# Kernel optimization log

Hardware: AMD Instinct MI355X
Metric: run time of the kernel (lower is better)

The kernel has to match this reference:

```python
import jax, jax.numpy as jnp
import numpy as np

HEAD_DIM = 128
NUM_HEADS = 16
CONTEXT_LENGTH = 4096
THETA_BASE = 10000.0


def precompute_rope(head_dim, context_length, theta_base=THETA_BASE):
    inv_freq = 1.0 / theta_base ** (jnp.arange(0, head_dim, 2, dtype=jnp.float32) / head_dim)
    positions = jnp.arange(context_length, dtype=jnp.float32)
    angles = positions[:, None] * inv_freq[None, :]          # [T, hd/2]
    angles = jnp.concatenate([angles, angles], axis=1)       # [T, hd]
    return jnp.cos(angles), jnp.sin(angles)


def apply_rope(x, cos, sin):
    # x: [b, h, s, hd]
    s, hd = x.shape[2], x.shape[3]
    x1, x2 = x[..., : hd // 2], x[..., hd // 2 :]
    rotated = jnp.concatenate([-x2, x1], axis=-1)
    return (x * cos[None, None, :s, :] + rotated * sin[None, None, :s, :]).astype(x.dtype)


def setup_inputs() -> dict:
    key = jax.random.key(0)
    ks = jax.random.split(key, 5)
    b, s, d = 2, 2048, 2048
    scale = 1.0 / np.sqrt(d)
    return {
        "x": jax.random.normal(ks[0], (b, s, d), dtype=jnp.float32),
        "Wq": jax.random.normal(ks[1], (d, d), dtype=jnp.float32) * scale,
        "Wk": jax.random.normal(ks[2], (d, d), dtype=jnp.float32) * scale,
        "Wv": jax.random.normal(ks[3], (d, d), dtype=jnp.float32) * scale,
        "Wo": jax.random.normal(ks[4], (d, d), dtype=jnp.float32) * scale,
    }


def reference(x, Wq, Wk, Wv, Wo):
    b, s, d = x.shape
    h, hd = NUM_HEADS, HEAD_DIM
    cos, sin = precompute_rope(hd, CONTEXT_LENGTH)

    q = (x @ Wq).reshape(b, s, h, hd).transpose(0, 2, 1, 3)  # [b,h,s,hd]
    k = (x @ Wk).reshape(b, s, h, hd).transpose(0, 2, 1, 3)
    v = (x @ Wv).reshape(b, s, h, hd).transpose(0, 2, 1, 3)

    q = apply_rope(q, cos, sin)
    k = apply_rope(k, cos, sin)

    scores = jnp.einsum("bhqd,bhkd->bhqk", q, k)             # [b,h,s,s]
    causal = jnp.tril(jnp.ones((s, s), dtype=bool))
    scores = jnp.where(causal[None, None], scores, -jnp.inf)
    weights = jax.nn.softmax(scores / np.sqrt(hd), axis=-1)
    ctx = jnp.einsum("bhqk,bhkd->bhqd", weights, v)          # [b,h,s,hd]
    ctx = ctx.transpose(0, 2, 1, 3).reshape(b, s, d)
    return ctx @ Wo
```

## Files before the change

### kernel.cpp

```cpp
#include <hip/hip_runtime.h>
#include <hip/hip_bf16.h>

typedef __attribute__((ext_vector_type(8))) __bf16 bf16x8;
typedef __attribute__((ext_vector_type(8))) short  short8;
typedef __attribute__((ext_vector_type(4))) float  f32x4;
typedef unsigned short u16;
typedef unsigned int   u32;

__device__ __forceinline__ u16 f2bf(float f) {
  u32 u = __builtin_bit_cast(u32, f);
  u += 0x7fffu + ((u >> 16) & 1u);
  return (u16)(u >> 16);
}
__device__ __forceinline__ float bf2f(u16 h) {
  return __builtin_bit_cast(float, (u32)h << 16);
}

#define MFMA_BF16(a, b, c) __builtin_amdgcn_mfma_f32_16x16x32_bf16( \
    __builtin_bit_cast(bf16x8, (a)), __builtin_bit_cast(bf16x8, (b)), (c), 0, 0, 0)

__device__ __forceinline__ void gload_lds16(const void* g, void* l) {
  __builtin_amdgcn_global_load_lds(
      (const __attribute__((address_space(1))) void*)g,
      (__attribute__((address_space(3))) void*)l, 16, 0, 0);
}

#define SEQ   2048
#define DMODEL 2048
#define NH    16
#define HD    128

static constexpr size_t SZ_MAT   = 4096ull * 2048 * 2;
static constexpr size_t OFF_XB   = 0;
static constexpr size_t OFF_WQKVT= OFF_XB   + SZ_MAT;
static constexpr size_t OFF_WOT  = OFF_WQKVT+ 3ull*2048*2048*2;
static constexpr size_t OFF_Q    = OFF_WOT  + 2048ull*2048*2;
static constexpr size_t OFF_K    = OFF_Q    + SZ_MAT;
static constexpr size_t OFF_VT   = OFF_K    + SZ_MAT;
static constexpr size_t OFF_CTX  = OFF_VT   + SZ_MAT;
static constexpr size_t OFF_COS  = OFF_CTX  + SZ_MAT;
static constexpr size_t OFF_SIN  = OFF_COS  + 2048ull*64*4;
static constexpr size_t WS_NEED  = OFF_SIN  + 2048ull*64*4;

__global__ void cast_x_kernel(const float* __restrict__ x, u16* __restrict__ xb, int n4) {
  int id = blockIdx.x * blockDim.x + threadIdx.x;
  if (id >= n4) return;
  float4 v = ((const float4*)x)[id];
  ushort4 o;
  o.x = f2bf(v.x); o.y = f2bf(v.y); o.z = f2bf(v.z); o.w = f2bf(v.w);
  ((ushort4*)xb)[id] = o;
}

__global__ void castT_w_kernel(const float* __restrict__ W0, const float* __restrict__ W1,
                               const float* __restrict__ W2, const float* __restrict__ W3,
                               u16* __restrict__ Wqkvt, u16* __restrict__ Wot) {
  __shared__ float tile[32][33];
  int z = blockIdx.z;
  const float* W = (z == 0) ? W0 : (z == 1) ? W1 : (z == 2) ? W2 : W3;
  u16* Out = (z < 3) ? (Wqkvt + (size_t)z * 2048 * 2048) : Wot;
  int n0 = blockIdx.x * 32, k0 = blockIdx.y * 32;
  int tx = threadIdx.x, ty = threadIdx.y;
  #pragma unroll
  for (int i = 0; i < 4; i++)
    tile[ty + 8 * i][tx] = W[(size_t)(k0 + ty + 8 * i) * 2048 + n0 + tx];
  __syncthreads();
  #pragma unroll
  for (int i = 0; i < 4; i++)
    Out[(size_t)(n0 + ty + 8 * i) * 2048 + k0 + tx] = f2bf(tile[tx][ty + 8 * i]);
}

__global__ void rope_table_kernel(float* __restrict__ ct, float* __restrict__ st) {
  int id = blockIdx.x * blockDim.x + threadIdx.x;
  int pos = id >> 6, j = id & 63;
  float inv = exp2f(-(float)j * (13.287712379549449f / 64.0f));
  float a = (float)pos * inv;
  ct[id] = cosf(a);
  st[id] = sinf(a);
}

__global__ void rope_apply_kernel(u16* __restrict__ Q, u16* __restrict__ K,
                                  const float* __restrict__ ct, const float* __restrict__ st) {
  int id = blockIdx.x * blockDim.x + threadIdx.x;
  u16* P = blockIdx.y ? K : Q;
  int row = id >> 10;
  int r = id & 1023;
  int hh = r >> 6, j = r & 63;
  int pos = row & 2047;
  size_t base = (size_t)row * 2048 + hh * 128 + j;
  float x1 = bf2f(P[base]), x2 = bf2f(P[base + 64]);
  float c = ct[pos * 64 + j], s = st[pos * 64 + j];
  P[base]      = f2bf(x1 * c - x2 * s);
  P[base + 64] = f2bf(x2 * c + x1 * s);
}

template <int EPI>
__global__ __launch_bounds__(256)
void gemm_bt_kernel(const u16* __restrict__ A, const u16* __restrict__ Bt,
                    u16* __restrict__ Qo, u16* __restrict__ Ko, u16* __restrict__ Vto,
                    float* __restrict__ Co, int K) {
  __shared__ u16 Al[128 * 32];
  __shared__ u16 Bl[128 * 32];
  const int tid = threadIdx.x;
  const int lane = tid & 63;
  const int w = tid >> 6;
  const int grp = lane >> 4, lr = lane & 15;
  const int bm = blockIdx.y, bn = blockIdx.x;
  const int wm = w >> 1, wn = w & 1;
  f32x4 acc[4][4] = {};
  const char* Ab = (const char*)(A + (size_t)bm * 128 * K);
  const char* Bb = (const char*)(Bt + (size_t)bn * 128 * K);
  const int c0 = tid, c1 = tid + 256;
  const int rA0 = c0 >> 2, cb0 = (c0 & 3) * 16;
  const int rA1 = c1 >> 2, cb1 = (c1 & 3) * 16;

  for (int kt = 0; kt < K; kt += 32) {
    gload_lds16(Ab + (size_t)rA0 * K * 2 + kt * 2 + cb0, (char*)Al + c0 * 16);
    gload_lds16(Ab + (size_t)rA1 * K * 2 + kt * 2 + cb1, (char*)Al + c1 * 16);
    gload_lds16(Bb + (size_t)rA0 * K * 2 + kt * 2 + cb0, (char*)Bl + c0 * 16);
    gload_lds16(Bb + (size_t)rA1 * K * 2 + kt * 2 + cb1, (char*)Bl + c1 * 16);
    __syncthreads();
    short8 af[4], bf[4];
    #pragma unroll
    for (int mi = 0; mi < 4; mi++)
      af[mi] = *(const short8*)(Al + (wm * 64 + mi * 16 + lr) * 32 + grp * 8);
    #pragma unroll
    for (int nj = 0; nj < 4; nj++)
      bf[nj] = *(const short8*)(Bl + (wn * 64 + nj * 16 + lr) * 32 + grp * 8);
    #pragma unroll
    for (int mi = 0; mi < 4; mi++)
      #pragma unroll
      for (int nj = 0; nj < 4; nj++)
        acc[mi][nj] = MFMA_BF16(af[mi], bf[nj], acc[mi][nj]);
    __syncthreads();
  }

  const int rowBase = bm * 128 + wm * 64 + grp * 4;
  if (EPI == 0) {
    const int seg = bn >> 4;
    const int colBase = (bn & 15) * 128 + wn * 64 + lr;
    if (seg < 2) {
      u16* O = seg ? Ko : Qo;
      #pragma unroll
      for (int mi = 0; mi < 4; mi++)
        #pragma unroll
        for (int nj = 0; nj < 4; nj++) {
          int col = colBase + nj * 16;
          int row = rowBase + mi * 16;
          #pragma unroll
          for (int r = 0; r < 4; r++)
            O[(size_t)(row + r) * 2048 + col] = f2bf(acc[mi][nj][r]);
        }
    } else {
      #pragma unroll
      for (int mi = 0; mi < 4; mi++) {
        int row = rowBase + mi * 16;
        int b = row >> 11, s = row & 2047;
        int sp = (s & ~31) | (((s >> 2) & 3) << 3) | (((s >> 4) & 1) << 2);
        #pragma unroll
        for (int nj = 0; nj < 4; nj++) {
          int colv = colBase + nj * 16;
          ushort4 o;
          o.x = f2bf(acc[mi][nj][0]); o.y = f2bf(acc[mi][nj][1]);
          o.z = f2bf(acc[mi][nj][2]); o.w = f2bf(acc[mi][nj][3]);
          *(ushort4*)(Vto + (size_t)(b * 2048 + colv) * 2048 + sp) = o;
        }
      }
    }
  } else {
    const int colBase = bn * 128 + wn * 64 + lr;
    #pragma unroll
    for (int mi = 0; mi < 4; mi++)
      #pragma unroll
      for (int nj = 0; nj < 4; nj++)
        #pragma unroll
        for (int r = 0; r < 4; r++)
          Co[(size_t)(rowBase + mi * 16 + r) * 2048 + colBase + nj * 16] = acc[mi][nj][r];
  }
}

__global__ __launch_bounds__(512, 4)
void attn_kernel(const u16* __restrict__ Q, const u16* __restrict__ K,
                 const u16* __restrict__ Vt, u16* __restrict__ ctx) {
  __shared__ u16 Kl[2][64 * 128];
  __shared__ u16 Vl[2][128 * 64];
  const int qt = blockIdx.x, bh = blockIdx.y;
  const int b = bh >> 4, h = bh & 15;
  const int tid = threadIdx.x;
  const int w = tid >> 6, lane = tid & 63;
  const int grp = lane >> 4, lr = lane & 15;
  const int q0w = qt * 128 + w * 16;
  const int qrow = q0w + lr;
  const u16* Qp = Q + ((size_t)(b * 2048 + qrow)) * 2048 + h * 128;
  short8 qf[4];
  #pragma unroll
  for (int kk = 0; kk < 4; kk++)
    qf[kk] = *(const short8*)(Qp + kk * 32 + grp * 8);

  f32x4 acc_o[8] = {};
  float m_run = -3.0e38f, l_run = 0.0f;
  const float ce = 0.08838834764831845f * 1.4426950408889634f;

  const char* Kbh = (const char*)K  + ((size_t)b * 2048 * 2048 + h * 128) * 2;
  const char* Vbh = (const char*)Vt + ((size_t)(b * 2048 + h * 128)) * 2048 * 2;

  auto stage = [&](int buf, int kvt) {
    const int kv0 = kvt * 64;
    #pragma unroll
    for (int u = 0; u < 2; u++) {
      int c = tid + u * 512;
      int row = c >> 4, slot = c & 15;
      gload_lds16(Kbh + (size_t)(kv0 + row) * 4096 + ((slot ^ (row & 7)) << 4),
                  (char*)Kl[buf] + c * 16);
    }
    #pragma unroll
    for (int u = 0; u < 2; u++) {
      int c = tid + u * 512;
      int dd = c >> 3, slot = c & 7;
      gload_lds16(Vbh + (size_t)dd * 4096 + kv0 * 2 + ((slot ^ (dd & 7)) << 4),
                  (char*)Vl[buf] + c * 16);
    }
  };

  const int nkv = 2 * qt + 2;
  stage(0, 0);
  __syncthreads();

  for (int kvt = 0; kvt < nkv; kvt++) {
    const int kv0 = kvt * 64;
    const int cur = kvt & 1;
    if (kvt + 1 < nkv) stage(cur ^ 1, kvt + 1);

    if (kv0 <= q0w + 15) {
      const char* Kc = (const char*)Kl[cur];
      const char* Vc = (const char*)Vl[cur];
      f32x4 sa[4] = {};
      #pragma unroll
      for (int kk = 0; kk < 4; kk++) {
        #pragma unroll
        for (int mi = 0; mi < 4; mi++) {
          const int krow = mi * 16 + lr;
          short8 kf = *(const short8*)(Kc + krow * 256 + (((kk * 4 + grp) ^ (krow & 7)) << 4));
          sa[mi] = MFMA_BF16(kf, qf[kk], sa[mi]);
        }
      }
      float tmax = -3.0e38f;
      const bool dg = (kv0 + 63 > qrow);
      #pragma unroll
      for (int mi = 0; mi < 4; mi++)
        #pragma unroll
        for (int r = 0; r < 4; r++) {
          float s = sa[mi][r];
          if (dg && (kv0 + mi * 16 + grp * 4 + r > qrow)) s = -3.0e38f;
          sa[mi][r] = s;
          tmax = fmaxf(tmax, s);
        }
      tmax = fmaxf(tmax, __shfl_xor(tmax, 16, 64));
      tmax = fmaxf(tmax, __shfl_xor(tmax, 32, 64));
      const float m_new = fmaxf(m_run, tmax);
      const float alpha = exp2f((m_run - m_new) * ce);
      float psum = 0.0f;
      #pragma unroll
      for (int mi = 0; mi < 4; mi++)
        #pragma unroll
        for (int r = 0; r < 4; r++) {
          float e = exp2f((sa[mi][r] - m_new) * ce);
          sa[mi][r] = e;
          psum += e;
        }
      psum += __shfl_xor(psum, 16, 64);
      psum += __shfl_xor(psum, 32, 64);
      l_run = l_run * alpha + psum;
      m_run = m_new;
      #pragma unroll
      for (int mi = 0; mi < 8; mi++) acc_o[mi] *= alpha;

      short8 pb[2];
      #pragma unroll
      for (int kb = 0; kb < 2; kb++)
        #pragma unroll
        for (int i = 0; i < 4; i++) {
          pb[kb][i]     = (short)f2bf(sa[2 * kb][i]);
          pb[kb][4 + i] = (short)f2bf(sa[2 * kb + 1][i]);
        }
      #pragma unroll
      for (int mi = 0; mi < 8; mi++) {
        const int vrow = mi * 16 + lr;
        #pragma unroll
        for (int kb = 0; kb < 2; kb++) {
          short8 vf = *(const short8*)(Vc + vrow * 128 + (((kb * 4 + grp) ^ (vrow & 7)) << 4));
          acc_o[mi] = MFMA_BF16(vf, pb[kb], acc_o[mi]);
        }
      }
    }
    __syncthreads();
  }

  const float inv_l = 1.0f / l_run;
  u16* Cp = ctx + ((size_t)(b * 2048 + qrow)) * 2048 + h * 128;
  #pragma unroll
  for (int mi = 0; mi < 8; mi++) {
    ushort4 o;
    o.x = f2bf(acc_o[mi][0] * inv_l);
    o.y = f2bf(acc_o[mi][1] * inv_l);
    o.z = f2bf(acc_o[mi][2] * inv_l);
    o.w = f2bf(acc_o[mi][3] * inv_l);
    *(ushort4*)(Cp + mi * 16 + grp * 4) = o;
  }
}

extern "C" void kernel_launch(void* const* d_in, const int* in_sizes, int n_in,
                              void* d_out, int out_size, void* d_ws, size_t ws_size,
                              hipStream_t stream) {
  const float* x  = (const float*)d_in[0];
  const float* Wq = (const float*)d_in[1];
  const float* Wk = (const float*)d_in[2];
  const float* Wv = (const float*)d_in[3];
  const float* Wo = (const float*)d_in[4];
  float* out = (float*)d_out;
  char* ws = (char*)d_ws;
  if (ws_size < WS_NEED) return;

  u16* xb    = (u16*)(ws + OFF_XB);
  u16* Wqkvt = (u16*)(ws + OFF_WQKVT);
  u16* Wot   = (u16*)(ws + OFF_WOT);
  u16* Qb    = (u16*)(ws + OFF_Q);
  u16* Kb    = (u16*)(ws + OFF_K);
  u16* Vtb   = (u16*)(ws + OFF_VT);
  u16* ctxb  = (u16*)(ws + OFF_CTX);
  float* ctab = (float*)(ws + OFF_COS);
  float* stab = (float*)(ws + OFF_SIN);

  cast_x_kernel<<<8192, 256, 0, stream>>>(x, xb, 2097152);
  castT_w_kernel<<<dim3(64, 64, 4), dim3(32, 8), 0, stream>>>(Wq, Wk, Wv, Wo, Wqkvt, Wot);
  rope_table_kernel<<<512, 256, 0, stream>>>(ctab, stab);
  gemm_bt_kernel<0><<<dim3(48, 32), 256, 0, stream>>>(xb, Wqkvt, Qb, Kb, Vtb, nullptr, 2048);
  rope_apply_kernel<<<dim3(16384, 2), 256, 0, stream>>>(Qb, Kb, ctab, stab);
  attn_kernel<<<dim3(16, 32), 512, 0, stream>>>(Qb, Kb, Vtb, ctxb);
  gemm_bt_kernel<1><<<dim3(16, 32), 256, 0, stream>>>(ctxb, Wot, nullptr, nullptr, nullptr, out, 2048);
}
```

Baseline: 463.9 us.

## Replace QKV projection GEMM with 256x256 double-buffered, swizzled 8-wave kernel

Adds a dedicated QKV GEMM using 256x256 block tiles, 512 threads, a 64-wide K step, XOR-swizzled LDS layout and double-buffered async global-to-LDS loads interleaved with MFMA phases under explicit barriers, vmcnt waits and priority hints. This is meant to raise data reuse and hide memory latency compared with the old 128x128 single-buffered tile that synchronised on every 32-wide K step. The output GEMM keeps the old kernel with the epilogue template removed. The trade-offs are a larger LDS footprint (128KB per block) and a grid of 384 blocks, which may leave the GPU unevenly loaded.

After: 445.2 us. 1.04x faster.

```diff
diff --git a/kernel.cpp b/kernel.cpp
--- a/kernel.cpp
+++ b/kernel.cpp
@@ -93,10 +93,152 @@
   P[base + 64] = f2bf(x2 * c + x1 * s);
 }
 
-template <int EPI>
+#define SB __builtin_amdgcn_sched_barrier(0)
+#define BAR()   do { SB; __builtin_amdgcn_s_barrier(); SB; } while (0)
+#define VMCNT4() do { SB; asm volatile("s_waitcnt vmcnt(4)" ::: "memory"); SB; } while (0)
+#define VMCNT0() do { SB; asm volatile("s_waitcnt vmcnt(0)" ::: "memory"); SB; } while (0)
+
+#define STAGE8(gb, kt, H, lb)                                                  \
+  do { _Pragma("unroll")                                                       \
+    for (int u = 0; u < 2; u++) {                                              \
+      int c = tid + u * 512;                                                   \
+      int rr = c >> 3, sl = c & 7;                                             \
+      gload_lds16((gb) + (size_t)((H) * 128 + rr) * 4096 + (size_t)(kt) * 128  \
+                       + ((sl ^ (rr & 7)) << 4),                               \
+                  (lb) + (H) * 16384 + c * 16);                                \
+    } } while (0)
+
+#define LDA8(lb, MG)                                                           \
+  do { _Pragma("unroll")                                                       \
+    for (int mi = 0; mi < 4; mi++) {                                           \
+      af[mi][0] = *(const short8*)((lb) + aoff + ((MG) + mi) * 2048 + sw0);    \
+      af[mi][1] = *(const short8*)((lb) + aoff + ((MG) + mi) * 2048 + sw1);    \
+    } } while (0)
+
+#define LDB4(lb, NG)                                                           \
+  do { _Pragma("unroll")                                                       \
+    for (int nj = 0; nj < 2; nj++) {                                           \
+      bfr[(NG) + nj][0] = *(const short8*)((lb) + boff + ((NG) + nj) * 2048 + sw0); \
+      bfr[(NG) + nj][1] = *(const short8*)((lb) + boff + ((NG) + nj) * 2048 + sw1); \
+    } } while (0)
+
+#define MMQ(MG, NG)                                                            \
+  do {                                                                         \
+    __builtin_amdgcn_s_setprio(1);                                             \
+    _Pragma("unroll")                                                          \
+    for (int mi = 0; mi < 4; mi++) {                                           \
+      _Pragma("unroll")                                                        \
+      for (int nj = 0; nj < 2; nj++) {                                         \
+        acc[(MG) + mi][(NG) + nj] =                                            \
+            MFMA_BF16(af[mi][0], bfr[(NG) + nj][0], acc[(MG) + mi][(NG) + nj]);\
+        acc[(MG) + mi][(NG) + nj] =                                            \
+            MFMA_BF16(af[mi][1], bfr[(NG) + nj][1], acc[(MG) + mi][(NG) + nj]);\
+      }                                                                        \
+    }                                                                          \
+    __builtin_amdgcn_s_setprio(0);                                             \
+  } while (0)
+
+#define GEMM8_ITER(K1v, K2v, K3v, LAST)                                        \
+  do {                                                                         \
+    LDA8(A0p, 0); LDB4(B0p, 0);                                                \
+    STAGE8(Ab, (K1v), 0, A1p);                                                 \
+    BAR(); MMQ(0, 0); BAR();                                                   \
+    LDB4(B0p, 2);                                                              \
+    STAGE8(Ab, (K1v), 1, A1p);                                                 \
+    BAR(); MMQ(0, 2); BAR();                                                   \
+    LDA8(A0p, 4);                                                              \
+    if (!(LAST)) STAGE8(Bb, (K2v), 0, B0p);                                    \
+    BAR(); MMQ(4, 2); BAR();                                                   \
+    if (!(LAST)) STAGE8(Ab, (K2v), 0, A0p);                                    \
+    if (LAST) { VMCNT0(); } else { VMCNT4(); }                                 \
+    BAR(); MMQ(4, 0); BAR();                                                   \
+    LDA8(A1p, 0); LDB4(B1p, 0);                                                \
+    if (!(LAST)) STAGE8(Ab, (K2v), 1, A0p);                                    \
+    BAR(); MMQ(0, 0); BAR();                                                   \
+    LDB4(B1p, 2);                                                              \
+    if (!(LAST)) STAGE8(Bb, (K2v), 1, B0p);                                    \
+    BAR(); MMQ(0, 2); BAR();                                                   \
+    LDA8(A1p, 4);                                                              \
+    if (!(LAST)) STAGE8(Bb, (K3v), 0, B1p);                                    \
+    BAR(); MMQ(4, 2); BAR();                                                   \
+    if (!(LAST)) { STAGE8(Bb, (K3v), 1, B1p); VMCNT4(); }                      \
+    BAR(); MMQ(4, 0); BAR();                                                   \
+  } while (0)
+
+__global__ __launch_bounds__(512, 2)
+void gemm8_qkv_kernel(const u16* __restrict__ A, const u16* __restrict__ Bt,
+                      u16* __restrict__ Qo, u16* __restrict__ Ko,
+                      u16* __restrict__ Vto) {
+  __shared__ u16 Asm[2][16384];
+  __shared__ u16 Bsm[2][16384];
+  const int tid = threadIdx.x;
+  const int lane = tid & 63, w = tid >> 6;
+  const int grp = lane >> 4, lr = lane & 15;
+  const int wm = w >> 2, wn = w & 3;
+  const int bm = blockIdx.y, bn = blockIdx.x;
+
+  const char* Ab = (const char*)A + (size_t)bm * 256 * 4096;
+  const char* Bb = (const char*)Bt + (size_t)bn * 256 * 4096;
+  char* A0p = (char*)Asm[0]; char* A1p = (char*)Asm[1];
+  char* B0p = (char*)Bsm[0]; char* B1p = (char*)Bsm[1];
+
+  f32x4 acc[8][4] = {};
+  short8 af[4][2], bfr[4][2];
+  const int aoff = wm * 16384 + lr * 128;
+  const int boff = wn * 8192 + lr * 128;
+  const int sw0 = ((grp    ) ^ (lr & 7)) << 4;
+  const int sw1 = ((grp + 4) ^ (lr & 7)) << 4;
+
+  STAGE8(Ab, 0, 0, A0p);
+  STAGE8(Ab, 0, 1, A0p);
+  STAGE8(Bb, 0, 0, B0p);
+  STAGE8(Bb, 0, 1, B0p);
+  STAGE8(Bb, 1, 0, B1p);
+  STAGE8(Bb, 1, 1, B1p);
+  VMCNT4();
+  BAR();
+
+  #pragma unroll 1
+  for (int t = 0; t < 15; ++t) {
+    GEMM8_ITER(2 * t + 1, 2 * t + 2, 2 * t + 3, false);
+  }
+  GEMM8_ITER(31, 0, 0, true);
+
+  const int seg = bn >> 3;
+  const int row0 = bm * 256 + wm * 128 + grp * 4;
+  const int col0 = (bn & 7) * 256 + wn * 64 + lr;
+  if (seg < 2) {
+    u16* O = seg ? Ko : Qo;
+    #pragma unroll
+    for (int ai = 0; ai < 8; ai++)
+      #pragma unroll
+      for (int nj = 0; nj < 4; nj++) {
+        int col = col0 + nj * 16;
+        int row = row0 + ai * 16;
+        #pragma unroll
+        for (int r = 0; r < 4; r++)
+          O[(size_t)(row + r) * 2048 + col] = f2bf(acc[ai][nj][r]);
+      }
+  } else {
+    #pragma unroll
+    for (int ai = 0; ai < 8; ai++) {
+      int row = row0 + ai * 16;
+      int b = row >> 11, s = row & 2047;
+      int sp = (s & ~31) | (((s >> 2) & 3) << 3) | (((s >> 4) & 1) << 2);
+      #pragma unroll
+      for (int nj = 0; nj < 4; nj++) {
+        int colv = col0 + nj * 16;
+        ushort4 o;
+        o.x = f2bf(acc[ai][nj][0]); o.y = f2bf(acc[ai][nj][1]);
+        o.z = f2bf(acc[ai][nj][2]); o.w = f2bf(acc[ai][nj][3]);
+        *(ushort4*)(Vto + (size_t)(b * 2048 + colv) * 2048 + sp) = o;
+      }
+    }
+  }
+}
+
 __global__ __launch_bounds__(256)
 void gemm_bt_kernel(const u16* __restrict__ A, const u16* __restrict__ Bt,
-                    u16* __restrict__ Qo, u16* __restrict__ Ko, u16* __restrict__ Vto,
                     float* __restrict__ Co, int K) {
   __shared__ u16 Al[128 * 32];
   __shared__ u16 Bl[128 * 32];
@@ -135,47 +277,14 @@
   }
 
   const int rowBase = bm * 128 + wm * 64 + grp * 4;
-  if (EPI == 0) {
-    const int seg = bn >> 4;
-    const int colBase = (bn & 15) * 128 + wn * 64 + lr;
-    if (seg < 2) {
-      u16* O = seg ? Ko : Qo;
-      #pragma unroll
-      for (int mi = 0; mi < 4; mi++)
-        #pragma unroll
-        for (int nj = 0; nj < 4; nj++) {
-          int col = colBase + nj * 16;
-          int row = rowBase + mi * 16;
-          #pragma unroll
-          for (int r = 0; r < 4; r++)
-            O[(size_t)(row + r) * 2048 + col] = f2bf(acc[mi][nj][r]);
-        }
-    } else {
-      #pragma unroll
-      for (int mi = 0; mi < 4; mi++) {
-        int row = rowBase + mi * 16;
-        int b = row >> 11, s = row & 2047;
-        int sp = (s & ~31) | (((s >> 2) & 3) << 3) | (((s >> 4) & 1) << 2);
-        #pragma unroll
-        for (int nj = 0; nj < 4; nj++) {
-          int colv = colBase + nj * 16;
-          ushort4 o;
-          o.x = f2bf(acc[mi][nj][0]); o.y = f2bf(acc[mi][nj][1]);
-          o.z = f2bf(acc[mi][nj][2]); o.w = f2bf(acc[mi][nj][3]);
-          *(ushort4*)(Vto + (size_t)(b * 2048 + colv) * 2048 + sp) = o;
-        }
-      }
-    }
-  } else {
-    const int colBase = bn * 128 + wn * 64 + lr;
-    #pragma unroll
-    for (int mi = 0; mi < 4; mi++)
-      #pragma unroll
-      for (int nj = 0; nj < 4; nj++)
-        #pragma unroll
-        for (int r = 0; r < 4; r++)
-          Co[(size_t)(rowBase + mi * 16 + r) * 2048 + colBase + nj * 16] = acc[mi][nj][r];
-  }
+  const int colBase = bn * 128 + wn * 64 + lr;
+  #pragma unroll
+  for (int mi = 0; mi < 4; mi++)
+    #pragma unroll
+    for (int nj = 0; nj < 4; nj++)
+      #pragma unroll
+      for (int r = 0; r < 4; r++)
+        Co[(size_t)(rowBase + mi * 16 + r) * 2048 + colBase + nj * 16] = acc[mi][nj][r];
 }
 
 __global__ __launch_bounds__(512, 4)
@@ -333,8 +442,8 @@
   cast_x_kernel<<<8192, 256, 0, stream>>>(x, xb, 2097152);
   castT_w_kernel<<<dim3(64, 64, 4), dim3(32, 8), 0, stream>>>(Wq, Wk, Wv, Wo, Wqkvt, Wot);
   rope_table_kernel<<<512, 256, 0, stream>>>(ctab, stab);
-  gemm_bt_kernel<0><<<dim3(48, 32), 256, 0, stream>>>(xb, Wqkvt, Qb, Kb, Vtb, nullptr, 2048);
+  gemm8_qkv_kernel<<<dim3(24, 16), 512, 0, stream>>>(xb, Wqkvt, Qb, Kb, Vtb);
   rope_apply_kernel<<<dim3(16384, 2), 256, 0, stream>>>(Qb, Kb, ctab, stab);
   attn_kernel<<<dim3(16, 32), 512, 0, stream>>>(Qb, Kb, Vtb, ctxb);
-  gemm_bt_kernel<1><<<dim3(16, 32), 256, 0, stream>>>(ctxb, Wot, nullptr, nullptr, nullptr, out, 2048);
-}
+  gemm_bt_kernel<<<dim3(16, 32), 256, 0, stream>>>(ctxb, Wot, out, 2048);
+}
```
